# Optimization experiments

Hardware: AMD Instinct MI355X
Metric: run time of the kernel (lower is better)

## Reference

```python
import jax, jax.numpy as jnp
from jax import lax
import numpy as np

TAG_NAMES = ["O", "B-MAT", "I-MAT", "B-PRO", "I-PRO", "B-APL", "I-APL", "B-SMT", "I-SMT", "B-CMT", "I-CMT", "B-DSC", "I-DSC"]
IMP = -100.0


def _init_crf_params(key):
    # torchcrf initializes uniform(-0.1, 0.1); CRF_NEW then clamps invalid
    # BIO transitions to -100 per define_invalid_crf_transitions/init_crf_transitions.
    K = len(TAG_NAMES)
    k1, k2, k3 = jax.random.split(key, 3)
    start = np.array(jax.random.uniform(k1, (K,), minval=-0.1, maxval=0.1), dtype=np.float32)
    end = np.array(jax.random.uniform(k2, (K,), minval=-0.1, maxval=0.1), dtype=np.float32)
    trans = np.array(jax.random.uniform(k3, (K, K), minval=-0.1, maxval=0.1), dtype=np.float32)
    pref = [t[0] for t in TAG_NAMES]
    ent = [t.split('-')[1] if '-' in t else '' for t in TAG_NAMES]
    for i in range(K):
        if pref[i] in ('B', 'I'):  # invalid begin/end for BIO
            start[i] = IMP
            end[i] = IMP
    for i in range(K):
        for j in range(K):
            # invalid_transitions_position: O -> I  (B->P, I->P are empty sets)
            if pref[i] == 'O' and pref[j] == 'I':
                trans[i, j] = IMP
            # invalid_transitions_tags: B->I, I->I across different entity types
            if pref[i] in ('B', 'I') and pref[j] == 'I' and ent[i] != ent[j]:
                trans[i, j] = IMP
    return jnp.asarray(start), jnp.asarray(end), jnp.asarray(trans)


def setup_inputs() -> dict:
    key = jax.random.key(0)
    k_em, k_tag, k_p = jax.random.split(key, 3)
    B, T, K = 4096, 512, len(TAG_NAMES)
    emissions = jax.random.normal(k_em, (B, T, K), dtype=jnp.float32)
    tags = jax.random.randint(k_tag, (B, T), 0, K, dtype=jnp.int64)
    mask = jnp.ones((B, T), dtype=bool)
    start_transitions, end_transitions, transitions = _init_crf_params(k_p)
    return {"emissions": emissions, "tags": tags, "mask": mask,
            "start_transitions": start_transitions,
            "end_transitions": end_transitions,
            "transitions": transitions}


def reference(emissions, tags, mask, start_transitions, end_transitions, transitions):
    # torchcrf CRF.forward with batch_first=True, reduction='sum':
    # returns sum over batch of log p(tags | emissions).
    B, T, K = emissions.shape
    maskf = mask.astype(emissions.dtype)

    # ---- numerator: score of the given tag path ----
    emit = jnp.take_along_axis(emissions, tags[..., None], axis=2)[..., 0]  # [B,T]
    trans = transitions[tags[:, :-1], tags[:, 1:]]                           # [B,T-1]
    num = start_transitions[tags[:, 0]] + emit[:, 0]
    num = num + jnp.sum((trans + emit[:, 1:]) * maskf[:, 1:], axis=1)
    seq_ends = jnp.sum(mask.astype(jnp.int32), axis=1) - 1                   # [B]
    last_tags = tags[jnp.arange(B), seq_ends]
    num = num + end_transitions[last_tags]

    # ---- denominator: log partition via forward-algorithm scan over time ----
    em_t = jnp.swapaxes(emissions, 0, 1)   # [T,B,K]
    mask_t = jnp.swapaxes(mask, 0, 1)      # [T,B]
    score0 = start_transitions + em_t[0]   # [B,K]

    def step(score, xs):
        em, m = xs  # em: [B,K], m: [B]
        # broadcast: [B,K_from,1] + [K_from,K_to] + [B,1,K_to]
        nxt = jax.nn.logsumexp(score[:, :, None] + transitions[None] + em[:, None, :], axis=1)
        return jnp.where(m[:, None], nxt, score), None

    score, _ = lax.scan(step, score0, (em_t[1:], mask_t[1:]))
    denom = jax.nn.logsumexp(score + end_transitions, axis=1)  # [B]

    return jnp.sum(num - denom)
```

## Files before the change

### kernel.cpp

```cpp
#include <hip/hip_runtime.h>


typedef float  f4  __attribute__((ext_vector_type(4)));
typedef float  f4u __attribute__((ext_vector_type(4), aligned(4)));
typedef short  s4  __attribute__((ext_vector_type(4)));
typedef int    i2  __attribute__((ext_vector_type(2)));

#define FENCE do { __builtin_amdgcn_sched_barrier(0); \
                   asm volatile("" ::: "memory"); } while (0)

__device__ __forceinline__ unsigned pack_bf16(float x, float y) {
  return __builtin_amdgcn_perm(__float_as_uint(y) + 0x8000u,
                               __float_as_uint(x) + 0x8000u, 0x07060302u);
}

__global__ void __launch_bounds__(128, 1)
crf_main(const float* __restrict__ em,
         const int*   __restrict__ tags,
         const float* __restrict__ startT,
         const float* __restrict__ endT,
         const float* __restrict__ trans,
         float* __restrict__ partial)
{
  __shared__ float ldsT[256];
  __shared__ float ldsS[16], ldsE[16];
  __shared__ float pFa[256];
  __shared__ float lsF[16], numF[16], resB[16];
  __shared__ int   tag255[16];

  const int tid = threadIdx.x;
  for (int i = tid; i < 169; i += 128) {
    const int r_ = i / 13, c_ = i - r_ * 13;
    ldsT[r_ * 16 + c_] = trans[i];
  }
  if (tid < 13) ldsS[tid] = startT[tid];
  if (tid >= 16 && tid < 29) ldsE[tid - 16] = endT[tid - 16];
  __syncthreads();

  const int lane = tid & 63;
  const int n    = lane & 15;
  const int q    = lane >> 4;
  const bool is_fwd = (tid < 64);
  const int seq  = blockIdx.x * 16 + n;
  const int loadBase = (q < 3) ? 4 * q : 9;
  const int lo       = (q < 3) ? 4 * q : 12;
  const unsigned span = (q < 3) ? 3u : 0u;
  const float* emP = em + (size_t)seq * 6656 + loadBase;
  const int*   tgP = tags + (size_t)seq * 512;

  s4 afrag;
  {
    float av[4];
#pragma unroll
    for (int i = 0; i < 4; ++i) {
      const int kk = 4 * q + i;
      av[i] = (kk < 13 && n < 13)
            ? __expf(is_fwd ? ldsT[kk * 16 + n] : ldsT[n * 16 + kk]) : 0.0f;
    }
    i2 ai = { (int)pack_bf16(av[0], av[1]), (int)pack_bf16(av[2], av[3]) };
    afrag = __builtin_bit_cast(s4, ai);
  }

  f4 D;
#pragma unroll
  for (int r = 0; r < 4; ++r) {
    const int m = 4 * q + r;
    D[r] = (m < 13) ? __expf(is_fwd ? ldsS[m] : ldsE[m]) : 0.0f;
  }

  float logscale = 0.0f, em_acc = 0.0f, trans_acc = 0.0f;
  float sDs0 = 0, sDs1 = 0, sDs2 = 0, sDs3 = 0;
  float start_t0 = 0.0f;
  int tg_hi = 0, tg_lo = 0, tg511 = 0;
  f4 eA[16], eB[16];
  int4 tA[4], tB[4];

#define TGV(TB, k) ((((k) & 3) == 0) ? TB[(k) >> 2].x : (((k) & 3) == 1) ? TB[(k) >> 2].y \
                  : (((k) & 3) == 2) ? TB[(k) >> 2].z : TB[(k) >> 2].w)

#define LOADC(EB, TB, TC) do {                                          \
    const int tc_ = (TC);                                               \
    _Pragma("unroll")                                                   \
    for (int k_ = 0; k_ < 16; ++k_)                                     \
      EB[k_] = *(const f4u*)(emP + (size_t)(tc_ + k_) * 13);            \
    _Pragma("unroll")                                                   \
    for (int g_ = 0; g_ < 4; ++g_)                                      \
      TB[g_] = *(const int4*)(tgP + tc_ + 4 * g_);                      \
  } while (0)

#define RENORM4() do {                                                  \
    float cm_ = fmaxf(fmaxf(Ds0, Ds1), fmaxf(Ds2, Ds3));                \
    cm_ = fmaxf(cm_, __shfl_xor(cm_, 16, 64));                          \
    cm_ = fmaxf(cm_, __shfl_xor(cm_, 32, 64));                          \
    const float rc_ = __builtin_amdgcn_rcpf(cm_);                       \
    Ds0 *= rc_; Ds1 *= rc_; Ds2 *= rc_; Ds3 *= rc_;                     \
    logscale += __logf(cm_);                                            \
  } while (0)

#define CORE(EM4, RN, TGVv) do {                                        \
    const float e0 = __expf((q == 3) ? (EM4).w : (EM4).x);              \
    const float e1 = __expf((EM4).y);                                   \
    const float e2 = __expf((EM4).z);                                   \
    const float e3 = __expf((EM4).w);                                   \
    Ds0 = D[0] * e0; Ds1 = D[1] * e1; Ds2 = D[2] * e2; Ds3 = D[3] * e3; \
    if (RN) RENORM4();                                                  \
    {                                                                   \
      const unsigned ur_ = (unsigned)((TGVv) - lo);                     \
      const int rr_ = (TGVv) - loadBase;                                \
      const float s01_ = (rr_ & 1) ? (EM4).y : (EM4).x;                 \
      const float s23_ = (rr_ & 1) ? (EM4).w : (EM4).z;                 \
      const float sv_  = (rr_ & 2) ? s23_ : s01_;                       \
      em_acc += (ur_ <= span) ? sv_ : 0.0f;                             \
    }                                                                   \
    {                                                                   \
      i2 bi_ = { (int)pack_bf16(Ds0, Ds1), (int)pack_bf16(Ds2, Ds3) };  \
      s4 bf_ = __builtin_bit_cast(s4, bi_);                             \
      D = __builtin_amdgcn_mfma_f32_16x16x16bf16_1k(                    \
              afrag, bf_, (f4){0.f, 0.f, 0.f, 0.f}, 0, 0, 0);           \
    }                                                                   \
  } while (0)

#define PROCF(EB, TB, FIRST, LAST) do {                                 \
    _Pragma("unroll")                                                   \
    for (int k = 0; k < 16; ++k) {                                      \
      const int tgv = TGV(TB, k);                                       \
      if (FIRST && k == 0) start_t0 = ldsS[tgv];                        \
      else {                                                            \
        const int pv = (k == 0) ? tg_hi : TGV(TB, k - 1);               \
        trans_acc += ldsT[pv * 16 + tgv];                               \
      }                                                                 \
      const f4 em4 = EB[k];                                             \
      float Ds0, Ds1, Ds2, Ds3;                                         \
      CORE(em4, (k == 7 || k == 15), tgv);                              \
      if (LAST && k == 15) { sDs0 = Ds0; sDs1 = Ds1; sDs2 = Ds2; sDs3 = Ds3; } \
    }                                                                   \
    tg_hi = TGV(TB, 15);                                                \
  } while (0)

#define PROCB(EB, TB, FIRST) do {                                       \
    if (FIRST) tg511 = TGV(TB, 15);                                     \
    else       trans_acc += ldsT[TGV(TB, 15) * 16 + tg_lo];             \
    _Pragma("unroll")                                                   \
    for (int kk = 0; kk < 16; ++kk) {                                   \
      const int k = 15 - kk;                                            \
      const int tgv = TGV(TB, k);                                       \
      if (k > 0) trans_acc += ldsT[TGV(TB, k - 1) * 16 + tgv];          \
      const f4 em4 = EB[k];                                             \
      float Ds0, Ds1, Ds2, Ds3;                                         \
      CORE(em4, (k == 8 || k == 0), tgv);                               \
    }                                                                   \
    tg_lo = TGV(TB, 0);                                                 \
  } while (0)

  if (is_fwd) {
    LOADC(eA, tA, 0); LOADC(eB, tB, 16); FENCE;
    PROCF(eA, tA, true, false);
    for (int it = 0; it < 7; ++it) {
      LOADC(eA, tA, 32 * it + 32); FENCE;
      PROCF(eB, tB, false, false);
      LOADC(eB, tB, 32 * it + 48); FENCE;
      PROCF(eA, tA, false, false);
    }
    FENCE;
    PROCF(eB, tB, false, true);
    float emr = em_acc + __shfl_xor(em_acc, 16, 64);
    emr += __shfl_xor(emr, 32, 64);
    if (q == 0) {
      lsF[n]    = logscale;
      numF[n]   = start_t0 + emr + trans_acc;
      tag255[n] = tg_hi;
    }
    *(f4*)&pFa[n * 16 + 4 * q] = (f4){sDs0, sDs1, sDs2, sDs3};
  } else {
    LOADC(eA, tA, 496); LOADC(eB, tB, 480); FENCE;
    PROCB(eA, tA, true);
    for (int it = 0; it < 7; ++it) {
      LOADC(eA, tA, 464 - 32 * it); FENCE;
      PROCB(eB, tB, false);
      LOADC(eB, tB, 448 - 32 * it); FENCE;
      PROCB(eA, tA, false);
    }
    FENCE;
    PROCB(eB, tB, false);
  }

  __syncthreads();

  if (!is_fwd) {
    const f4 al = *(const f4*)&pFa[n * 16 + 4 * q];
    float z = al[0] * D[0] + al[1] * D[1] + al[2] * D[2] + al[3] * D[3];
    z += __shfl_xor(z, 16, 64);
    z += __shfl_xor(z, 32, 64);
    float emr = em_acc + __shfl_xor(em_acc, 16, 64);
    emr += __shfl_xor(emr, 32, 64);
    const float denom = lsF[n] + logscale + __logf(z);
    const float num   = numF[n] + emr + trans_acc
                      + ldsT[tag255[n] * 16 + tg_lo]
                      + ldsE[tg511];
    if (q == 0) resB[n] = num - denom;
  }
  __syncthreads();
  if (tid == 0) {
    float s = 0.0f;
#pragma unroll
    for (int i = 0; i < 16; ++i) s += resB[i];
    partial[blockIdx.x] = s;
  }

#undef TGV
#undef LOADC
#undef RENORM4
#undef CORE
#undef PROCF
#undef PROCB
}

__global__ void __launch_bounds__(256)
crf_reduce(const float* __restrict__ part, float* __restrict__ out, int n)
{
  float v = 0.0f;
  for (int i = threadIdx.x; i < n; i += 256) v += part[i];
#pragma unroll
  for (int off = 32; off > 0; off >>= 1) v += __shfl_down(v, off);
  __shared__ float w[4];
  if ((threadIdx.x & 63) == 0) w[threadIdx.x >> 6] = v;
  __syncthreads();
  if (threadIdx.x == 0) out[0] = (w[0] + w[1]) + (w[2] + w[3]);
}

extern "C" void kernel_launch(void* const* d_in, const int* in_sizes, int n_in,
                              void* d_out, int out_size, void* d_ws, size_t ws_size,
                              hipStream_t stream) {
  const float* em   = (const float*)d_in[0];
  const int*   tags = (const int*)d_in[1];
  const float* st   = (const float*)d_in[3];
  const float* en   = (const float*)d_in[4];
  const float* tr   = (const float*)d_in[5];
  float* part = (float*)d_ws;

  crf_main<<<256, 128, 0, stream>>>(em, tags, st, en, tr, part);
  crf_reduce<<<1, 256, 0, stream>>>(part, (float*)d_out, 256);
}
```

Measured before the change: 187.8 us.

## Stage emissions through LDS with async global-to-LDS DMA and halve sequences per block

Replaces per-lane unaligned global vector loads of emissions and tags with coalesced global_load_lds DMA into double-buffered LDS tiles, then reads f4 fragments from LDS. Each block now handles 8 sequences instead of 16 (only half of the MFMA columns are useful), and the grid doubles to 512 blocks so more CUs run concurrently. This targets poor coalescing and register pressure from the 32-element register prefetch, at the cost of wasting half the MFMA lanes, adding LDS traffic, and relying on manual vmcnt waits.

```diff
diff --git a/kernel.cpp b/kernel.cpp
--- a/kernel.cpp
+++ b/kernel.cpp
@@ -1,18 +1,24 @@
 #include <hip/hip_runtime.h>
 
 
-typedef float  f4  __attribute__((ext_vector_type(4)));
-typedef float  f4u __attribute__((ext_vector_type(4), aligned(4)));
-typedef short  s4  __attribute__((ext_vector_type(4)));
-typedef int    i2  __attribute__((ext_vector_type(2)));
-
-#define FENCE do { __builtin_amdgcn_sched_barrier(0); \
-                   asm volatile("" ::: "memory"); } while (0)
+typedef float f4 __attribute__((ext_vector_type(4)));
+typedef short s4 __attribute__((ext_vector_type(4)));
+typedef int   i2 __attribute__((ext_vector_type(2)));
+
+#define AS1 __attribute__((address_space(1)))
+#define AS3 __attribute__((address_space(3)))
+typedef unsigned int u32;
 
 __device__ __forceinline__ unsigned pack_bf16(float x, float y) {
   return __builtin_amdgcn_perm(__float_as_uint(y) + 0x8000u,
                                __float_as_uint(x) + 0x8000u, 0x07060302u);
 }
+__device__ __forceinline__ void dma4(const float* g, float* l) {
+  __builtin_amdgcn_global_load_lds((const AS1 u32*)g, (AS3 u32*)l, 4, 0, 0);
+}
+#define WAITV18 asm volatile("s_waitcnt vmcnt(18)" ::: "memory")
+#define WAITV0  asm volatile("s_waitcnt vmcnt(0)"  ::: "memory")
+#define LGKM0   asm volatile("s_waitcnt lgkmcnt(0)" ::: "memory")
 
 __global__ void __launch_bounds__(128, 1)
 crf_main(const float* __restrict__ em,
@@ -22,16 +28,17 @@
          const float* __restrict__ trans,
          float* __restrict__ partial)
 {
-  __shared__ float ldsT[256];
-  __shared__ float ldsS[16], ldsE[16];
-  __shared__ float pFa[256];
-  __shared__ float lsF[16], numF[16], resB[16];
-  __shared__ int   tag255[16];
+  __shared__ __align__(16) float emBuf[2][2][1088];
+  __shared__ __align__(16) int   tgBuf[2][2][64];
+  __shared__ float ldsT[256], ldsS[16], ldsE[16];
+  __shared__ float pFa[8][16];
+  __shared__ float lsF[8], numF[8], resB[8];
+  __shared__ int   tag255s[8];
 
   const int tid = threadIdx.x;
   for (int i = tid; i < 169; i += 128) {
-    const int r_ = i / 13, c_ = i - r_ * 13;
-    ldsT[r_ * 16 + c_] = trans[i];
+    const int r = i / 13, c = i - r * 13;
+    ldsT[r * 16 + c] = trans[i];
   }
   if (tid < 13) ldsS[tid] = startT[tid];
   if (tid >= 16 && tid < 29) ldsE[tid - 16] = endT[tid - 16];
@@ -39,14 +46,22 @@
 
   const int lane = tid & 63;
   const int n    = lane & 15;
+  const int n8   = n & 7;
   const int q    = lane >> 4;
-  const bool is_fwd = (tid < 64);
-  const int seq  = blockIdx.x * 16 + n;
-  const int loadBase = (q < 3) ? 4 * q : 9;
-  const int lo       = (q < 3) ? 4 * q : 12;
-  const unsigned span = (q < 3) ? 3u : 0u;
-  const float* emP = em + (size_t)seq * 6656 + loadBase;
-  const int*   tgP = tags + (size_t)seq * 512;
+  const int wid  = tid >> 6;
+  const bool is_fwd = (wid == 0);
+
+  int emOff[17];
+#pragma unroll
+  for (int d = 0; d < 17; ++d) {
+    const int wd = d * 64 + lane;
+    const int s  = wd / 136;
+    const int rem = wd - s * 136;
+    int tt = rem >> 4; if (tt > 7) tt = 7;
+    int st = rem & 15; if (st > 12) st = 12;
+    emOff[d] = (blockIdx.x * 8 + s) * 6656 + tt * 13 + st;
+  }
+  const int tgOff = (blockIdx.x * 8 + (lane >> 3)) * 512 + (lane & 7);
 
   s4 afrag;
   {
@@ -60,7 +75,6 @@
     i2 ai = { (int)pack_bf16(av[0], av[1]), (int)pack_bf16(av[2], av[3]) };
     afrag = __builtin_bit_cast(s4, ai);
   }
-
   f4 D;
 #pragma unroll
   for (int r = 0; r < 4; ++r) {
@@ -68,151 +82,169 @@
     D[r] = (m < 13) ? __expf(is_fwd ? ldsS[m] : ldsE[m]) : 0.0f;
   }
 
-  float logscale = 0.0f, em_acc = 0.0f, trans_acc = 0.0f;
+  float* bufE0 = emBuf[wid][0]; float* bufE1 = emBuf[wid][1];
+  int*   bufT0 = tgBuf[wid][0]; int*   bufT1 = tgBuf[wid][1];
+  const int off = (q < 3) ? 4 * q : 12;
+
+  float logscale = 0, em_acc = 0, trans_acc = 0, start_t0 = 0;
+  int tg_hi = 0, tg_lo = 0, tg511 = 0;
+  f4 emA[8], emB[8];
+  int4 tqA[2], tqB[2];
   float sDs0 = 0, sDs1 = 0, sDs2 = 0, sDs3 = 0;
-  float start_t0 = 0.0f;
-  int tg_hi = 0, tg_lo = 0, tg511 = 0;
-  f4 eA[16], eB[16];
-  int4 tA[4], tB[4];
-
-#define TGV(TB, k) ((((k) & 3) == 0) ? TB[(k) >> 2].x : (((k) & 3) == 1) ? TB[(k) >> 2].y \
-                  : (((k) & 3) == 2) ? TB[(k) >> 2].z : TB[(k) >> 2].w)
-
-#define LOADC(EB, TB, TC) do {                                          \
-    const int tc_ = (TC);                                               \
-    _Pragma("unroll")                                                   \
-    for (int k_ = 0; k_ < 16; ++k_)                                     \
-      EB[k_] = *(const f4u*)(emP + (size_t)(tc_ + k_) * 13);            \
-    _Pragma("unroll")                                                   \
-    for (int g_ = 0; g_ < 4; ++g_)                                      \
-      TB[g_] = *(const int4*)(tgP + tc_ + 4 * g_);                      \
-  } while (0)
-
-#define RENORM4() do {                                                  \
-    float cm_ = fmaxf(fmaxf(Ds0, Ds1), fmaxf(Ds2, Ds3));                \
-    cm_ = fmaxf(cm_, __shfl_xor(cm_, 16, 64));                          \
-    cm_ = fmaxf(cm_, __shfl_xor(cm_, 32, 64));                          \
-    const float rc_ = __builtin_amdgcn_rcpf(cm_);                       \
-    Ds0 *= rc_; Ds1 *= rc_; Ds2 *= rc_; Ds3 *= rc_;                     \
-    logscale += __logf(cm_);                                            \
-  } while (0)
-
-#define CORE(EM4, RN, TGVv) do {                                        \
-    const float e0 = __expf((q == 3) ? (EM4).w : (EM4).x);              \
-    const float e1 = __expf((EM4).y);                                   \
-    const float e2 = __expf((EM4).z);                                   \
-    const float e3 = __expf((EM4).w);                                   \
-    Ds0 = D[0] * e0; Ds1 = D[1] * e1; Ds2 = D[2] * e2; Ds3 = D[3] * e3; \
-    if (RN) RENORM4();                                                  \
-    {                                                                   \
-      const unsigned ur_ = (unsigned)((TGVv) - lo);                     \
-      const int rr_ = (TGVv) - loadBase;                                \
-      const float s01_ = (rr_ & 1) ? (EM4).y : (EM4).x;                 \
-      const float s23_ = (rr_ & 1) ? (EM4).w : (EM4).z;                 \
-      const float sv_  = (rr_ & 2) ? s23_ : s01_;                       \
-      em_acc += (ur_ <= span) ? sv_ : 0.0f;                             \
-    }                                                                   \
-    {                                                                   \
-      i2 bi_ = { (int)pack_bf16(Ds0, Ds1), (int)pack_bf16(Ds2, Ds3) };  \
-      s4 bf_ = __builtin_bit_cast(s4, bi_);                             \
-      D = __builtin_amdgcn_mfma_f32_16x16x16bf16_1k(                    \
-              afrag, bf_, (f4){0.f, 0.f, 0.f, 0.f}, 0, 0, 0);           \
-    }                                                                   \
-  } while (0)
-
-#define PROCF(EB, TB, FIRST, LAST) do {                                 \
-    _Pragma("unroll")                                                   \
-    for (int k = 0; k < 16; ++k) {                                      \
-      const int tgv = TGV(TB, k);                                       \
-      if (FIRST && k == 0) start_t0 = ldsS[tgv];                        \
-      else {                                                            \
-        const int pv = (k == 0) ? tg_hi : TGV(TB, k - 1);               \
-        trans_acc += ldsT[pv * 16 + tgv];                               \
-      }                                                                 \
-      const f4 em4 = EB[k];                                             \
-      float Ds0, Ds1, Ds2, Ds3;                                         \
-      CORE(em4, (k == 7 || k == 15), tgv);                              \
-      if (LAST && k == 15) { sDs0 = Ds0; sDs1 = Ds1; sDs2 = Ds2; sDs3 = Ds3; } \
-    }                                                                   \
-    tg_hi = TGV(TB, 15);                                                \
-  } while (0)
-
-#define PROCB(EB, TB, FIRST) do {                                       \
-    if (FIRST) tg511 = TGV(TB, 15);                                     \
-    else       trans_acc += ldsT[TGV(TB, 15) * 16 + tg_lo];             \
-    _Pragma("unroll")                                                   \
-    for (int kk = 0; kk < 16; ++kk) {                                   \
-      const int k = 15 - kk;                                            \
-      const int tgv = TGV(TB, k);                                       \
-      if (k > 0) trans_acc += ldsT[TGV(TB, k - 1) * 16 + tgv];          \
-      const f4 em4 = EB[k];                                             \
-      float Ds0, Ds1, Ds2, Ds3;                                         \
-      CORE(em4, (k == 8 || k == 0), tgv);                               \
-    }                                                                   \
-    tg_lo = TGV(TB, 0);                                                 \
+
+#define ISSUE(RB, BE, BT) do {                                         \
+    const float* _er = em + (size_t)(RB) * 13;                         \
+    _Pragma("unroll")                                                  \
+    for (int d_ = 0; d_ < 17; ++d_) dma4(_er + emOff[d_], (BE) + 64 * d_); \
+    dma4((const float*)(tags + (RB) + tgOff), (float*)(BT));           \
+  } while (0)
+
+#define READC(BE, BT, ER, TQ) do {                                     \
+    _Pragma("unroll")                                                  \
+    for (int t_ = 0; t_ < 8; ++t_)                                     \
+      ER[t_] = *(const f4*)&(BE)[n8 * 136 + t_ * 16 + off];            \
+    TQ[0] = *(const int4*)&(BT)[n8 * 8];                               \
+    TQ[1] = *(const int4*)&(BT)[n8 * 8 + 4];                           \
+  } while (0)
+
+#define TG8(TQ, k) ((k) < 4 ? ((k)==0?TQ[0].x:(k)==1?TQ[0].y:(k)==2?TQ[0].z:TQ[0].w) \
+                            : ((k)==4?TQ[1].x:(k)==5?TQ[1].y:(k)==6?TQ[1].z:TQ[1].w))
+
+#define RENORM4() do {                                                 \
+    float cm_ = fmaxf(fmaxf(Ds0, Ds1), fmaxf(Ds2, Ds3));               \
+    cm_ = fmaxf(cm_, __shfl_xor(cm_, 16, 64));                         \
+    cm_ = fmaxf(cm_, __shfl_xor(cm_, 32, 64));                         \
+    const float rc_ = __builtin_amdgcn_rcpf(cm_);                      \
+    Ds0 *= rc_; Ds1 *= rc_; Ds2 *= rc_; Ds3 *= rc_;                    \
+    logscale += __logf(cm_);                                           \
+  } while (0)
+
+#define CORE(EM4, RN, TG, SAVE) do {                                   \
+    const f4 _e4 = (EM4);                                              \
+    const float e0 = __expf(_e4.x), e1 = __expf(_e4.y),                \
+                e2 = __expf(_e4.z), e3 = __expf(_e4.w);                \
+    float Ds0 = D[0]*e0, Ds1 = D[1]*e1, Ds2 = D[2]*e2, Ds3 = D[3]*e3;  \
+    if (RN) RENORM4();                                                 \
+    { const int dd = (TG) - 4 * q;                                     \
+      const float v01 = (dd & 1) ? _e4.y : _e4.x;                      \
+      const float v23 = (dd & 1) ? _e4.w : _e4.z;                      \
+      const float vv  = (dd & 2) ? v23 : v01;                          \
+      em_acc += ((unsigned)dd <= 3u) ? vv : 0.0f; }                    \
+    if (SAVE) { sDs0 = Ds0; sDs1 = Ds1; sDs2 = Ds2; sDs3 = Ds3; }      \
+    { i2 bi_ = { (int)pack_bf16(Ds0, Ds1), (int)pack_bf16(Ds2, Ds3) }; \
+      D = __builtin_amdgcn_mfma_f32_16x16x16bf16_1k(                   \
+              afrag, __builtin_bit_cast(s4, bi_),                      \
+              (f4){0.f, 0.f, 0.f, 0.f}, 0, 0, 0); }                    \
+  } while (0)
+
+#define BKF(TQ, C) do {                                                \
+    if ((C) == 0) start_t0 = ldsS[TG8(TQ, 0)];                         \
+    else trans_acc += ldsT[tg_hi * 16 + TG8(TQ, 0)];                   \
+    _Pragma("unroll")                                                  \
+    for (int k_ = 1; k_ < 8; ++k_)                                     \
+      trans_acc += ldsT[TG8(TQ, k_ - 1) * 16 + TG8(TQ, k_)];           \
+    tg_hi = TG8(TQ, 7);                                                \
+  } while (0)
+
+#define BKB(TQ, C) do {                                                \
+    if ((C) == 0) tg511 = TG8(TQ, 7);                                  \
+    else trans_acc += ldsT[TG8(TQ, 7) * 16 + tg_lo];                   \
+    _Pragma("unroll")                                                  \
+    for (int k_ = 0; k_ < 7; ++k_)                                     \
+      trans_acc += ldsT[TG8(TQ, k_) * 16 + TG8(TQ, k_ + 1)];           \
+    tg_lo = TG8(TQ, 0);                                                \
+  } while (0)
+
+#define COMPF(ER, TQ, C) do {                                          \
+    _Pragma("unroll")                                                  \
+    for (int k_ = 0; k_ < 8; ++k_)                                     \
+      CORE(ER[k_], (k_ == 7), TG8(TQ, k_), ((C) == 31 && k_ == 7));    \
+  } while (0)
+
+#define COMPB(ER, TQ) do {                                             \
+    _Pragma("unroll")                                                  \
+    for (int kk_ = 0; kk_ < 8; ++kk_) {                                \
+      const int k_ = 7 - kk_;                                          \
+      CORE(ER[k_], (kk_ == 7), TG8(TQ, k_), false);                    \
+    }                                                                  \
   } while (0)
 
   if (is_fwd) {
-    LOADC(eA, tA, 0); LOADC(eB, tB, 16); FENCE;
-    PROCF(eA, tA, true, false);
-    for (int it = 0; it < 7; ++it) {
-      LOADC(eA, tA, 32 * it + 32); FENCE;
-      PROCF(eB, tB, false, false);
-      LOADC(eB, tB, 32 * it + 48); FENCE;
-      PROCF(eA, tA, false, false);
-    }
-    FENCE;
-    PROCF(eB, tB, false, true);
+    ISSUE(0, bufE0, bufT0);
+    ISSUE(8, bufE1, bufT1);
+    WAITV18;
+    READC(bufE0, bufT0, emA, tqA);
+    for (int c = 0; c < 32; c += 2) {
+      LGKM0;
+      if (c < 30) { ISSUE(8 * (c + 2), bufE0, bufT0); WAITV18; } else WAITV0;
+      BKF(tqA, c);
+      READC(bufE1, bufT1, emB, tqB);
+      COMPF(emA, tqA, c);
+      LGKM0;
+      if (c < 29) { ISSUE(8 * (c + 3), bufE1, bufT1); WAITV18; } else WAITV0;
+      BKF(tqB, c + 1);
+      if (c < 30) READC(bufE0, bufT0, emA, tqA);
+      COMPF(emB, tqB, c + 1);
+    }
     float emr = em_acc + __shfl_xor(em_acc, 16, 64);
     emr += __shfl_xor(emr, 32, 64);
-    if (q == 0) {
-      lsF[n]    = logscale;
-      numF[n]   = start_t0 + emr + trans_acc;
-      tag255[n] = tg_hi;
-    }
-    *(f4*)&pFa[n * 16 + 4 * q] = (f4){sDs0, sDs1, sDs2, sDs3};
+    if (n < 8) {
+      *(f4*)&pFa[n8][4 * q] = (f4){sDs0, sDs1, sDs2, sDs3};
+      if (q == 0) {
+        lsF[n8] = logscale;
+        numF[n8] = start_t0 + emr + trans_acc;
+        tag255s[n8] = tg_hi;
+      }
+    }
+    __syncthreads();
+    __syncthreads();
   } else {
-    LOADC(eA, tA, 496); LOADC(eB, tB, 480); FENCE;
-    PROCB(eA, tA, true);
-    for (int it = 0; it < 7; ++it) {
-      LOADC(eA, tA, 464 - 32 * it); FENCE;
-      PROCB(eB, tB, false);
-      LOADC(eB, tB, 448 - 32 * it); FENCE;
-      PROCB(eA, tA, false);
-    }
-    FENCE;
-    PROCB(eB, tB, false);
-  }
-
-  __syncthreads();
-
-  if (!is_fwd) {
-    const f4 al = *(const f4*)&pFa[n * 16 + 4 * q];
-    float z = al[0] * D[0] + al[1] * D[1] + al[2] * D[2] + al[3] * D[3];
+    ISSUE(504, bufE0, bufT0);
+    ISSUE(496, bufE1, bufT1);
+    WAITV18;
+    READC(bufE0, bufT0, emA, tqA);
+    for (int c = 0; c < 32; c += 2) {
+      LGKM0;
+      if (c < 30) { ISSUE(504 - 8 * (c + 2), bufE0, bufT0); WAITV18; } else WAITV0;
+      BKB(tqA, c);
+      READC(bufE1, bufT1, emB, tqB);
+      COMPB(emA, tqA);
+      LGKM0;
+      if (c < 29) { ISSUE(504 - 8 * (c + 3), bufE1, bufT1); WAITV18; } else WAITV0;
+      BKB(tqB, c + 1);
+      if (c < 30) READC(bufE0, bufT0, emA, tqA);
+      COMPB(emB, tqB);
+    }
+    __syncthreads();
+    const f4 al = *(const f4*)&pFa[n8][4 * q];
+    float z = al.x * D[0] + al.y * D[1] + al.z * D[2] + al.w * D[3];
     z += __shfl_xor(z, 16, 64);
     z += __shfl_xor(z, 32, 64);
     float emr = em_acc + __shfl_xor(em_acc, 16, 64);
     emr += __shfl_xor(emr, 32, 64);
-    const float denom = lsF[n] + logscale + __logf(z);
-    const float num   = numF[n] + emr + trans_acc
-                      + ldsT[tag255[n] * 16 + tg_lo]
+    const float denom = lsF[n8] + logscale + __logf(z);
+    const float num   = numF[n8] + emr + trans_acc
+                      + ldsT[tag255s[n8] * 16 + tg_lo]
                       + ldsE[tg511];
-    if (q == 0) resB[n] = num - denom;
-  }
-  __syncthreads();
+    if (q == 0 && n < 8) resB[n8] = num - denom;
+    __syncthreads();
+  }
   if (tid == 0) {
     float s = 0.0f;
 #pragma unroll
-    for (int i = 0; i < 16; ++i) s += resB[i];
+    for (int i = 0; i < 8; ++i) s += resB[i];
     partial[blockIdx.x] = s;
   }
 
-#undef TGV
-#undef LOADC
+#undef ISSUE
+#undef READC
+#undef TG8
 #undef RENORM4
 #undef CORE
-#undef PROCF
-#undef PROCB
+#undef BKF
+#undef BKB
+#undef COMPF
+#undef COMPB
 }
 
 __global__ void __launch_bounds__(256)
@@ -221,7 +253,7 @@
   float v = 0.0f;
   for (int i = threadIdx.x; i < n; i += 256) v += part[i];
 #pragma unroll
-  for (int off = 32; off > 0; off >>= 1) v += __shfl_down(v, off);
+  for (int o = 32; o > 0; o >>= 1) v += __shfl_down(v, o);
   __shared__ float w[4];
   if ((threadIdx.x & 63) == 0) w[threadIdx.x >> 6] = v;
   __syncthreads();
@@ -238,6 +270,6 @@
   const float* tr   = (const float*)d_in[5];
   float* part = (float*)d_ws;
 
-  crf_main<<<256, 128, 0, stream>>>(em, tags, st, en, tr, part);
-  crf_reduce<<<1, 256, 0, stream>>>(part, (float*)d_out, 256);
-}
+  crf_main<<<512, 128, 0, stream>>>(em, tags, st, en, tr, part);
+  crf_reduce<<<1, 256, 0, stream>>>(part, (float*)d_out, 512);
+}
```

Result: slower. 207.1 us (+10.3%).
